# Kernel optimization log

Measured on AMD Instinct MI355X. Metric: run time of the kernel, lower is better.

The kernel has to match this reference:

```python
import jax, jax.numpy as jnp
import numpy as np

B, T, D, H, C = 32, 512, 768, 512, 7


def setup_inputs() -> dict:
    key = jax.random.key(0)
    ks = jax.random.split(key, 10)
    g = lambda k, shape: jax.random.normal(k, shape, jnp.float32) * 0.02
    return {
        "x": jax.random.normal(ks[0], (B, T, D), jnp.float32),
        # PyTorch LSTM params; b = b_ih + b_hh folded into one bias (same math)
        "Wf_ih": g(ks[1], (4 * H, 2 * D)),
        "Wf_hh": g(ks[2], (4 * H, H)),
        "bf": jnp.zeros((4 * H,), jnp.float32),
        "Wb_ih": g(ks[3], (4 * H, 2 * D)),
        "Wb_hh": g(ks[4], (4 * H, H)),
        "bb": jnp.zeros((4 * H,), jnp.float32),
        "W_enc": g(ks[5], (H, D)),
        "b_enc": jnp.zeros((H,), jnp.float32),
        "W_dec": g(ks[6], (H, H)),
        "b_dec": jnp.zeros((H,), jnp.float32),
        "v": jax.random.uniform(ks[7], (H,), jnpp := jnp.float32) if False else jax.random.uniform(ks[7], (H,), jnp.float32),
        "W_head": g(ks[8], (C, 2 * H)),
        "b_head": jnp.zeros((C,), jnp.float32),
    }


def reference(x, Wf_ih, Wf_hh, bf, Wb_ih, Wb_hh, bb, W_enc, b_enc, W_dec, b_dec, v, W_head, b_head):
    hid = W_dec.shape[0]
    # encoder projection is time-invariant -> hoist out of the loop (same math as original)
    enc_proj = jnp.einsum('btd,hd->bth', x, W_enc) + b_enc  # (B,T,H)

    def run_direction(x_seq, Wih, Whh, b):
        def step(carry, xt):
            h, c = carry                                    # (B,H) each
            dec = h @ W_dec.T + b_dec                       # (B,H)
            scores = jnp.tanh(enc_proj + dec[:, None, :]) @ v  # (B,T)
            w = jax.nn.softmax(scores, axis=1)
            ctx = jnp.einsum('bt,btd->bd', w, x)            # (B,D)
            inp = jnp.concatenate([ctx, xt], axis=1)        # (B,2D)
            gates = inp @ Wih.T + h @ Whh.T + b             # (B,4H), torch order i,f,g,o
            i_, f_, g_, o_ = jnp.split(gates, 4, axis=1)
            c = jax.nn.sigmoid(f_) * c + jax.nn.sigmoid(i_) * jnp.tanh(g_)
            h = jax.nn.sigmoid(o_) * jnp.tanh(c)
            return (h, c), h

        h0 = jnp.zeros((x.shape[0], hid), x.dtype)
        (_, _), hs = jax.lax.scan(step, (h0, h0), x_seq)
        return hs                                           # (T,B,H)

    x_seq = jnp.swapaxes(x, 0, 1)                           # (T,B,D)
    hs_f = run_direction(x_seq, Wf_ih, Wf_hh, bf)
    hs_b = run_direction(x_seq[::-1], Wb_ih, Wb_hh, bb)[::-1]
    comb = jnp.swapaxes(jnp.concatenate([hs_f, hs_b], axis=-1), 0, 1)  # (B,T,2H)
    return comb @ W_head.T + b_head                          # (B,T,C)
```

## Files before the change

### kernel.cpp

```cpp
#include <hip/hip_runtime.h>
#include <cstdint>
#include <cstddef>

#define L2E 1.4426950408889634f

typedef __attribute__((ext_vector_type(8))) short short8v;
typedef __attribute__((ext_vector_type(4))) float f32x4;
typedef unsigned long long ull;

__device__ __forceinline__ float fexp2(float x){ return __builtin_amdgcn_exp2f(x); }
__device__ __forceinline__ float frcp(float x){ return __builtin_amdgcn_rcpf(x); }
__device__ __forceinline__ float tanh_f(float x){
  return 1.f - 2.f*frcp(1.f + fexp2(2.f*L2E*x));
}
__device__ __forceinline__ float sigm_f(float x){
  return frcp(1.f + fexp2(-L2E*x));
}
__device__ __forceinline__ float bf2f(ushort u){ return __uint_as_float(((uint32_t)u)<<16); }
__device__ __forceinline__ ushort f2bf(float f){
  uint32_t x = __float_as_uint(f);
  uint32_t r = (x + 0x7FFFu + ((x>>16)&1u)) >> 16;
  return (ushort)r;
}

__device__ __forceinline__ float ld4f(const float* p){
  return __hip_atomic_load((float*)p, __ATOMIC_RELAXED, __HIP_MEMORY_SCOPE_AGENT);
}
__device__ __forceinline__ void st4f(float* p, float v){
  __hip_atomic_store(p, v, __ATOMIC_RELAXED, __HIP_MEMORY_SCOPE_AGENT);
}
__device__ __forceinline__ float2 ld8f(const float* p){
  union { ull u; float2 f; } c;
  c.u = __hip_atomic_load((ull*)p, __ATOMIC_RELAXED, __HIP_MEMORY_SCOPE_AGENT);
  return c.f;
}
__device__ __forceinline__ short8v ld16h(const ushort* p){
  union { ull u[2]; short8v s; } c;
  c.u[0] = __hip_atomic_load((ull*)p,     __ATOMIC_RELAXED, __HIP_MEMORY_SCOPE_AGENT);
  c.u[1] = __hip_atomic_load((ull*)(p+4), __ATOMIC_RELAXED, __HIP_MEMORY_SCOPE_AGENT);
  return c.s;
}
__device__ __forceinline__ void st8u(ushort* p, ull v){
  __hip_atomic_store((ull*)p, v, __ATOMIC_RELAXED, __HIP_MEMORY_SCOPE_AGENT);
}

namespace {
constexpr int NB = 32, TT = 512, DD = 768, HH = 512;
constexpr size_t EPB  = 0;
constexpr size_t XBB  = EPB  + (size_t)NB*HH*TT*2;
constexpr size_t HSB  = XBB  + (size_t)NB*TT*DD*2;
constexpr size_t WPKB = HSB  + (size_t)2*TT*NB*HH*2;
constexpr size_t WDPB = WPKB + (size_t)2*128*64*64*8*2;
constexpr size_t UCTXB= WDPB + (size_t)32*16*64*8*2;
constexpr size_t ZBB  = UCTXB+ (size_t)2*NB*DD*4;
constexpr size_t DECB = ZBB  + (size_t)2*NB*4;
constexpr size_t CSTB = DECB + (size_t)2*NB*HH*4;
constexpr size_t GSYB = CSTB + (size_t)2*NB*HH*4;
constexpr size_t WS_BYTES = GSYB + 32768;

constexpr int EPL  = 0;
constexpr int WPL  = 65536;
constexpr int REDL = 131072;
constexpr int DC2L = 147456;
constexpr int VSML = 151552;
constexpr int SCRL = 153600;
constexpr int EVSL = 157696;
constexpr int GFNL = 158208;
constexpr int LDS_BYTES = GFNL + 2176;
}

__device__ __forceinline__ void bar_arrive(uint* flags, uint token, int bid){
  __syncthreads();
  if (threadIdx.x == 0)
    __hip_atomic_store(&flags[bid*16], token, __ATOMIC_RELAXED, __HIP_MEMORY_SCOPE_AGENT);
}
__device__ __forceinline__ void bar_wait(uint* flags, uint token){
  if (threadIdx.x < 256) {
    while (__hip_atomic_load(&flags[threadIdx.x*16], __ATOMIC_RELAXED, __HIP_MEMORY_SCOPE_AGENT) < token)
      __builtin_amdgcn_s_sleep(1);
  }
  __syncthreads();
  asm volatile("" ::: "memory");
}

__global__ void k_xcast(const float* __restrict__ x, ushort* __restrict__ xb)
{
  size_t i = ((size_t)blockIdx.x*256 + threadIdx.x)*8;
  float4 v0 = *(const float4*)(x + i);
  float4 v1 = *(const float4*)(x + i + 4);
  short8v o;
  o[0]=(short)f2bf(v0.x); o[1]=(short)f2bf(v0.y); o[2]=(short)f2bf(v0.z); o[3]=(short)f2bf(v0.w);
  o[4]=(short)f2bf(v1.x); o[5]=(short)f2bf(v1.y); o[6]=(short)f2bf(v1.z); o[7]=(short)f2bf(v1.w);
  *(short8v*)(xb + i) = o;
}

__global__ void k_encproj(const float* __restrict__ x, const float* __restrict__ Wenc,
                          const float* __restrict__ benc, ushort* __restrict__ epT)
{
  int b = blockIdx.z, h0 = blockIdx.y*64, t0 = blockIdx.x*64;
  __shared__ float As[64][33];
  __shared__ float Bs[64][33];
  int tid = threadIdx.x;
  int n = tid & 63, mg = tid >> 6;
  float acc[16];
  #pragma unroll
  for (int j = 0; j < 16; j++) acc[j] = 0.f;
  int lr = tid >> 2, lk = (tid & 3) * 8;
  for (int k0 = 0; k0 < 768; k0 += 32) {
    const float* ap = Wenc + (size_t)(h0 + lr)*768 + k0 + lk;
    #pragma unroll
    for (int i = 0; i < 8; i++) As[lr][lk + i] = ap[i];
    const float* bp = x + ((size_t)b*512 + t0 + lr)*768 + k0 + lk;
    #pragma unroll
    for (int i = 0; i < 8; i++) Bs[lr][lk + i] = bp[i];
    __syncthreads();
    #pragma unroll
    for (int kk = 0; kk < 32; kk++) {
      float bv = Bs[n][kk];
      #pragma unroll
      for (int j = 0; j < 16; j++) acc[j] += As[mg*16 + j][kk] * bv;
    }
    __syncthreads();
  }
  #pragma unroll
  for (int j = 0; j < 16; j++) {
    int h = h0 + mg*16 + j;
    epT[((size_t)b*512 + h)*512 + t0 + n] = f2bf(acc[j] + benc[h]);
  }
}

__global__ void k_wpack(const float* __restrict__ Wfih, const float* __restrict__ Wfhh,
                        const float* __restrict__ Wbih, const float* __restrict__ Wbhh,
                        ushort* __restrict__ wpk)
{
  size_t f = (size_t)blockIdx.x*256 + threadIdx.x;
  int lane = (int)(f & 63), kstep = (int)((f>>6)&63), jblk = (int)((f>>12)&127), dir = (int)(f>>19);
  const float* Whh = dir ? Wbhh : Wfhh;
  const float* Wih = dir ? Wbih : Wfih;
  int c = lane & 15, gate = c >> 2, jj = c & 3;
  int row = gate*512 + jblk*4 + jj;
  int kbase = kstep*32 + (lane>>4)*8;
  short8v o;
  #pragma unroll
  for (int i = 0; i < 8; i++) {
    int k = kbase + i;
    float w = (k < 512) ? Whh[(size_t)row*512 + k] : Wih[(size_t)row*1536 + (k - 512)];
    o[i] = (short)f2bf(w);
  }
  *(short8v*)(wpk + f*8) = o;
}

__global__ void k_wdpack(const float* __restrict__ Wdec, ushort* __restrict__ wdp)
{
  int f = blockIdx.x*256 + threadIdx.x;
  int lane = f & 63, kstep = (f >> 6) & 15, nb = f >> 10;
  int n = nb*16 + (lane & 15);
  int kbase = kstep*32 + (lane >> 4)*8;
  short8v o;
  #pragma unroll
  for (int i = 0; i < 8; i++) o[i] = (short)f2bf(Wdec[(size_t)n*512 + kbase + i]);
  *(short8v*)(wdp + (size_t)f*8) = o;
}

__device__ __forceinline__ void gates_hx(int s, int wid, int lane, int l15, int lk8, int dirG,
    const ushort* __restrict__ hsb, const ushort* __restrict__ xb,
    const ushort* wpk_l, float* RED)
{
  if (wid >= 2 && wid <= 4) return;
  int b0 = l15, b1 = 16 + l15;
  f32x4 acc0 = {0,0,0,0}, acc1 = {0,0,0,0};
  if (wid < 2) {
    if (s > 0) {
      int t_prev = dirG ? (512 - s) : (s - 1);
      const ushort* h0 = hsb + (((size_t)dirG*512 + t_prev)*32 + b0)*512;
      const ushort* h1 = hsb + (((size_t)dirG*512 + t_prev)*32 + b1)*512;
      #pragma unroll
      for (int kk = 0; kk < 8; kk++) {
        int kstep = wid*8 + kk;
        int ko = kstep*32 + lk8;
        short8v a0v = ld16h(h0 + ko);
        short8v a1v = ld16h(h1 + ko);
        short8v bv  = *(const short8v*)(wpk_l + (size_t)kstep*512 + lane*8);
        acc0 = __builtin_amdgcn_mfma_f32_16x16x32_bf16(a0v, bv, acc0, 0, 0, 0);
        acc1 = __builtin_amdgcn_mfma_f32_16x16x32_bf16(a1v, bv, acc1, 0, 0, 0);
      }
    }
  } else {
    int t_in = dirG ? (511 - s) : s;
    const ushort* x0 = xb + ((size_t)b0*512 + t_in)*768;
    const ushort* x1 = xb + ((size_t)b1*512 + t_in)*768;
    #pragma unroll
    for (int kk = 0; kk < 8; kk++) {
      int kstep = wid*8 + kk;
      int ko = kstep*32 - 1280 + lk8;
      short8v a0v = __builtin_nontemporal_load((const short8v*)(x0 + ko));
      short8v a1v = __builtin_nontemporal_load((const short8v*)(x1 + ko));
      short8v bv  = *(const short8v*)(wpk_l + (size_t)kstep*512 + lane*8);
      acc0 = __builtin_amdgcn_mfma_f32_16x16x32_bf16(a0v, bv, acc0, 0, 0, 0);
      acc1 = __builtin_amdgcn_mfma_f32_16x16x32_bf16(a1v, bv, acc1, 0, 0, 0);
    }
  }
  int rr = (lane >> 4) * 4;
  #pragma unroll
  for (int r = 0; r < 4; r++) RED[((size_t)wid*32 + rr + r)*16 + l15] = acc0[r];
  #pragma unroll
  for (int r = 0; r < 4; r++) RED[((size_t)wid*32 + 16 + rr + r)*16 + l15] = acc1[r];
}

__global__ __launch_bounds__(512, 1) void k_loop(
    ushort* __restrict__ hsb, const ushort* __restrict__ xb, const ushort* __restrict__ ep,
    const ushort* __restrict__ wpk, const ushort* __restrict__ wdp,
    float* __restrict__ uctx, float* __restrict__ Zb, float* __restrict__ dec,
    float* __restrict__ cst, const float* __restrict__ bdec, const float* __restrict__ vg,
    const float* __restrict__ bfv, const float* __restrict__ bbv,
    uint* __restrict__ flags)
{
  extern __shared__ __align__(16) char dsm[];
  ushort* ep_l  = (ushort*)(dsm + EPL);
  ushort* wpk_l = (ushort*)(dsm + WPL);
  float*  RED   = (float*)(dsm + REDL);
  float*  DEC2  = (float*)(dsm + DC2L);
  float*  VSM   = (float*)(dsm + VSML);
  float*  SCRS  = (float*)(dsm + SCRL);
  float*  EVS   = (float*)(dsm + EVSL);
  float*  GFIN  = (float*)(dsm + GFNL);

  const int bid = blockIdx.x;
  const int tid = threadIdx.x;
  const int wid = tid >> 6, lane = tid & 63;
  const int l15 = lane & 15, lk8 = (lane >> 4) * 8;
  const int bS = bid >> 3, t0 = (bid & 7) * 64;
  const int dirG = bid >> 7, jblkG = bid & 127;
  uint bar_t = 0;

  {
    const ushort* esrc = ep + ((size_t)bS*512)*512 + t0;
    for (int i = tid; i < 4096; i += 512) {
      int h = i >> 3, c = i & 7;
      *(short8v*)(ep_l + h*64 + c*8) = *(const short8v*)(esrc + (size_t)h*512 + c*8);
    }
    const ushort* wsrc = wpk + (((size_t)dirG*128 + jblkG)*64)*512;
    for (int i = tid; i < 4096; i += 512)
      ((short8v*)wpk_l)[i] = ((const short8v*)wsrc)[i];
    VSM[tid] = vg[tid];
  }
  __syncthreads();

  for (int s = 0; s < TT; ++s) {
    if (bid < 32) {
      int nb = bid;
      if (s == 0) {
        for (int e = tid; e < 1024; e += 512) {
          int row = e >> 4, col = e & 15;
          st4f(dec + (size_t)row*512 + nb*16 + col, bdec[nb*16 + col]);
        }
      } else {
        f32x4 acc[4] = {{0,0,0,0},{0,0,0,0},{0,0,0,0},{0,0,0,0}};
        int tp0 = s - 1, tp1 = 512 - s;
        #pragma unroll
        for (int kk = 0; kk < 2; kk++) {
          int kstep = wid*2 + kk;
          int ko = kstep*32 + lk8;
          short8v bv = *(const short8v*)(wdp + (((size_t)nb*16 + kstep)*64 + lane)*8);
          #pragma unroll
          for (int m = 0; m < 4; m++) {
            int dir = m >> 1, brow = (m & 1)*16 + l15;
            int tp = dir ? tp1 : tp0;
            short8v av = ld16h(hsb + (((size_t)dir*512 + tp)*32 + brow)*512 + ko);
            acc[m] = __builtin_amdgcn_mfma_f32_16x16x32_bf16(av, bv, acc[m], 0, 0, 0);
          }
        }
        int rr = (lane >> 4) * 4;
        #pragma unroll
        for (int pass = 0; pass < 2; pass++) {
          #pragma unroll
          for (int mh = 0; mh < 2; mh++)
            #pragma unroll
            for (int r = 0; r < 4; r++)
              RED[((size_t)wid*32 + mh*16 + rr + r)*16 + l15] = acc[pass*2 + mh][r];
          __syncthreads();
          {
            int row = tid >> 4, col = tid & 15;
            float dv = 0.f;
            #pragma unroll
            for (int w = 0; w < 8; w++) dv += RED[((size_t)w*32 + row)*16 + col];
            st4f(dec + ((size_t)pass*32 + row)*512 + nb*16 + col, dv + bdec[nb*16 + col]);
          }
          __syncthreads();
        }
      }
    } else if (bid < 64) {
      int base = (bid - 32)*512 + tid;
      for (int i = base; i < 2*32*768; i += 16384) st4f(uctx + i, 0.f);
      if (base < 64) st4f(Zb + base, 0.f);
    }
    ++bar_t; bar_arrive(flags, bar_t, bid);
    gates_hx(s, wid, lane, l15, lk8, dirG, hsb, xb, wpk_l, RED);
    bar_wait(flags, bar_t);

    {
      DEC2[tid]       = ld4f(dec + (size_t)bS*512 + tid);
      DEC2[512 + tid] = ld4f(dec + ((size_t)32 + bS)*512 + tid);
      __syncthreads();
      int tl = tid & 63, hg = tid >> 6;
      float s0 = 0.f, s1 = 0.f;
      #pragma unroll 8
      for (int hh = 0; hh < 64; hh++) {
        int h = hg*64 + hh;
        float e = bf2f(ep_l[(size_t)h*64 + tl]);
        float vv = VSM[h];
        s0 += tanh_f(e + DEC2[h]) * vv;
        s1 += tanh_f(e + DEC2[512 + h]) * vv;
      }
      SCRS[((size_t)0*8 + hg)*64 + tl] = s0;
      SCRS[((size_t)1*8 + hg)*64 + tl] = s1;
      __syncthreads();
      if (tid < 128) {
        int dq = tid >> 6, tq = tid & 63;
        float sv = 0.f;
        #pragma unroll
        for (int g = 0; g < 8; g++) sv += SCRS[((size_t)dq*8 + g)*64 + tq];
        sv = fminf(sv, 100.f);
        float e = fexp2((sv - 32.f)*L2E);
        EVS[dq*64 + tq] = e;
        float z = e;
        #pragma unroll
        for (int off = 32; off; off >>= 1) z += __shfl_xor(z, off);
        if (tq == 0) unsafeAtomicAdd(Zb + dq*32 + bS, z);
      }
      __syncthreads();
      for (int dd = tid; dd < 768; dd += 512) {
        const ushort* xp = xb + ((size_t)bS*512 + t0)*768 + dd;
        float a0 = 0.f, a1 = 0.f;
        #pragma unroll 8
        for (int t = 0; t < 64; t++) {
          float xv = bf2f(xp[(size_t)t*768]);
          a0 += EVS[t]*xv;
          a1 += EVS[64 + t]*xv;
        }
        unsafeAtomicAdd(uctx + (size_t)bS*768 + dd, a0);
        unsafeAtomicAdd(uctx + ((size_t)32 + bS)*768 + dd, a1);
      }
    }
    ++bar_t; bar_arrive(flags, bar_t, bid);
    bar_wait(flags, bar_t);

    {
      if (wid >= 2 && wid <= 4) {
        int b0 = l15, b1 = 16 + l15;
        f32x4 acc0 = {0,0,0,0}, acc1 = {0,0,0,0};
        float zi0 = 1.0f / ld4f(Zb + dirG*32 + b0);
        float zi1 = 1.0f / ld4f(Zb + dirG*32 + b1);
        const float* u0 = uctx + ((size_t)dirG*32 + b0)*768;
        const float* u1 = uctx + ((size_t)dirG*32 + b1)*768;
        #pragma unroll
        for (int kk = 0; kk < 8; kk++) {
          int kstep = wid*8 + kk;
          int ko = kstep*32 - 512 + lk8;
          float2 xa = ld8f(u0 + ko),     xc = ld8f(u0 + ko + 2);
          float2 xe = ld8f(u0 + ko + 4), xg = ld8f(u0 + ko + 6);
          float2 ya = ld8f(u1 + ko),     yc = ld8f(u1 + ko + 2);
          float2 ye = ld8f(u1 + ko + 4), yg = ld8f(u1 + ko + 6);
          short8v a0v, a1v;
          a0v[0]=(short)f2bf(xa.x*zi0); a0v[1]=(short)f2bf(xa.y*zi0);
          a0v[2]=(short)f2bf(xc.x*zi0); a0v[3]=(short)f2bf(xc.y*zi0);
          a0v[4]=(short)f2bf(xe.x*zi0); a0v[5]=(short)f2bf(xe.y*zi0);
          a0v[6]=(short)f2bf(xg.x*zi0); a0v[7]=(short)f2bf(xg.y*zi0);
          a1v[0]=(short)f2bf(ya.x*zi1); a1v[1]=(short)f2bf(ya.y*zi1);
          a1v[2]=(short)f2bf(yc.x*zi1); a1v[3]=(short)f2bf(yc.y*zi1);
          a1v[4]=(short)f2bf(ye.x*zi1); a1v[5]=(short)f2bf(ye.y*zi1);
          a1v[6]=(short)f2bf(yg.x*zi1); a1v[7]=(short)f2bf(yg.y*zi1);
          short8v bv = *(const short8v*)(wpk_l + (size_t)kstep*512 + lane*8);
          acc0 = __builtin_amdgcn_mfma_f32_16x16x32_bf16(a0v, bv, acc0, 0, 0, 0);
          acc1 = __builtin_amdgcn_mfma_f32_16x16x32_bf16(a1v, bv, acc1, 0, 0, 0);
        }
        int rr = (lane >> 4) * 4;
        #pragma unroll
        for (int r = 0; r < 4; r++) RED[((size_t)wid*32 + rr + r)*16 + l15] = acc0[r];
        #pragma unroll
        for (int r = 0; r < 4; r++) RED[((size_t)wid*32 + 16 + rr + r)*16 + l15] = acc1[r];
      }
      __syncthreads();
      {
        int bb = tid >> 4, c = tid & 15;
        float g = 0.f;
        #pragma unroll
        for (int w = 0; w < 8; w++) g += RED[((size_t)w*32 + bb)*16 + c];
        GFIN[bb*17 + c] = g;
      }
      __syncthreads();
      if (tid < 32) {
        int b = tid;
        int j0 = jblkG*4;
        const float* bias = dirG ? bbv : bfv;
        size_t ci0 = ((size_t)dirG*32 + b)*512 + j0;
        float4 co = *(const float4*)&cst[ci0];
        float cold[4] = {co.x, co.y, co.z, co.w};
        float4 cn4;
        ull hp = 0;
        #pragma unroll
        for (int jj = 0; jj < 4; jj++) {
          int j = j0 + jj;
          float gi  = GFIN[b*17 + jj]       + bias[j];
          float gf  = GFIN[b*17 + 4 + jj]   + bias[512 + j];
          float gg  = GFIN[b*17 + 8 + jj]   + bias[1024 + j];
          float go_ = GFIN[b*17 + 12 + jj]  + bias[1536 + j];
          float cn = sigm_f(gf)*cold[jj] + sigm_f(gi)*tanh_f(gg);
          float h  = sigm_f(go_)*tanh_f(cn);
          ((float*)&cn4)[jj] = cn;
          hp |= ((ull)f2bf(h)) << (16*jj);
        }
        *(float4*)&cst[ci0] = cn4;
        int tw = dirG ? (511 - s) : s;
        st8u(hsb + (((size_t)dirG*512 + tw)*32 + b)*512 + j0, hp);
      }
    }
    ++bar_t; bar_arrive(flags, bar_t, bid);
    bar_wait(flags, bar_t);
  }
}

__global__ void k_head(const ushort* __restrict__ hsb, const float* __restrict__ Wh,
                       const float* __restrict__ bh, float* __restrict__ out)
{
  int wid = threadIdx.x >> 6, lane = threadIdx.x & 63;
  int r = blockIdx.x*4 + wid;
  int b = r >> 9, t = r & 511;
  float acc[7];
  #pragma unroll
  for (int c = 0; c < 7; c++) acc[c] = 0.f;
  const ushort* hf = hsb + (((size_t)t)*32 + b)*512;
  const ushort* hb = hsb + (((size_t)512 + t)*32 + b)*512;
  for (int k0 = 0; k0 < 512; k0 += 64) {
    int k = k0 + lane;
    float a = bf2f(hf[k]), bvv = bf2f(hb[k]);
    #pragma unroll
    for (int c = 0; c < 7; c++)
      acc[c] += a*Wh[c*1024 + k] + bvv*Wh[c*1024 + 512 + k];
  }
  #pragma unroll
  for (int c = 0; c < 7; c++) {
    float sres = acc[c];
    #pragma unroll
    for (int off = 32; off; off >>= 1) sres += __shfl_xor(sres, off);
    if (lane == c) out[((size_t)b*512 + t)*7 + c] = sres + bh[c];
  }
}

extern "C" void kernel_launch(void* const* d_in, const int* in_sizes, int n_in,
                              void* d_out, int out_size, void* d_ws, size_t ws_size,
                              hipStream_t stream) {
  (void)in_sizes; (void)n_in; (void)out_size;
  const float* x    = (const float*)d_in[0];
  const float* Wfih = (const float*)d_in[1];
  const float* Wfhh = (const float*)d_in[2];
  const float* bfv  = (const float*)d_in[3];
  const float* Wbih = (const float*)d_in[4];
  const float* Wbhh = (const float*)d_in[5];
  const float* bbv  = (const float*)d_in[6];
  const float* Wenc = (const float*)d_in[7];
  const float* benc = (const float*)d_in[8];
  const float* Wdec = (const float*)d_in[9];
  const float* bdec = (const float*)d_in[10];
  const float* v    = (const float*)d_in[11];
  const float* Whead= (const float*)d_in[12];
  const float* bhead= (const float*)d_in[13];
  float* out = (float*)d_out;
  char* ws = (char*)d_ws;

  if (ws_size < WS_BYTES) return;

  ushort* ep   = (ushort*)(ws + EPB);
  ushort* xb   = (ushort*)(ws + XBB);
  ushort* hsb  = (ushort*)(ws + HSB);
  ushort* wpk  = (ushort*)(ws + WPKB);
  ushort* wdp  = (ushort*)(ws + WDPB);
  float*  uctx = (float*)(ws + UCTXB);
  float*  Zb   = (float*)(ws + ZBB);
  float*  dec  = (float*)(ws + DECB);
  float*  cst  = (float*)(ws + CSTB);
  uint*   flags= (uint*)(ws + GSYB);

  hipFuncSetAttribute(reinterpret_cast<const void*>(k_loop),
                      hipFuncAttributeMaxDynamicSharedMemorySize, LDS_BYTES);

  hipMemsetAsync(ws + CSTB, 0, (size_t)2*NB*HH*4, stream);
  hipMemsetAsync(ws + GSYB, 0, 32768, stream);

  hipLaunchKernelGGL(k_xcast, dim3(6144), dim3(256), 0, stream, x, xb);
  hipLaunchKernelGGL(k_encproj, dim3(8,8,32), dim3(256), 0, stream, x, Wenc, benc, ep);
  hipLaunchKernelGGL(k_wpack, dim3(4096), dim3(256), 0, stream, Wfih, Wfhh, Wbih, Wbhh, wpk);
  hipLaunchKernelGGL(k_wdpack, dim3(128), dim3(256), 0, stream, Wdec, wdp);

  void* args[] = {
    (void*)&hsb, (void*)&xb, (void*)&ep, (void*)&wpk, (void*)&wdp,
    (void*)&uctx, (void*)&Zb, (void*)&dec, (void*)&cst,
    (void*)&bdec, (void*)&v, (void*)&bfv, (void*)&bbv, (void*)&flags
  };
  hipLaunchCooperativeKernel(reinterpret_cast<void*>(k_loop), dim3(256), dim3(512),
                             args, LDS_BYTES, stream);

  hipLaunchKernelGGL(k_head, dim3(4096), dim3(256), 0, stream, hsb, Whead, bhead, out);
}
```

Before: 15.48 ms.

## Repartition attention by hidden chunks with group-local sync, drop a grid barrier

Each block now owns a 64-wide hidden chunk for one batch row instead of a 64-step time slice. It computes its slice of the decoder projection redundantly, writes partial attention scores, and syncs only with the 8 blocks of its batch through new group flags. Those blocks then do the softmax and context reduction locally and write a normalized bf16 context, which removes one grid-wide barrier per step along with the global atomics on uctx and Zb. The cost is redundant decoder-projection work done with scalar FMAs instead of MFMA, and a global scratch buffer that aliases the encoder-projection region after it has been copied into LDS.

Result: slower. 16.11 ms (+4.0%).

```diff
diff --git a/kernel.cpp b/kernel.cpp
--- a/kernel.cpp
+++ b/kernel.cpp
@@ -29,10 +29,8 @@
 __device__ __forceinline__ void st4f(float* p, float v){
   __hip_atomic_store(p, v, __ATOMIC_RELAXED, __HIP_MEMORY_SCOPE_AGENT);
 }
-__device__ __forceinline__ float2 ld8f(const float* p){
-  union { ull u; float2 f; } c;
-  c.u = __hip_atomic_load((ull*)p, __ATOMIC_RELAXED, __HIP_MEMORY_SCOPE_AGENT);
-  return c.f;
+__device__ __forceinline__ void st2h(ushort* p, ushort v){
+  __hip_atomic_store(p, v, __ATOMIC_RELAXED, __HIP_MEMORY_SCOPE_AGENT);
 }
 __device__ __forceinline__ short8v ld16h(const ushort* p){
   union { ull u[2]; short8v s; } c;
@@ -61,11 +59,12 @@
 constexpr int EPL  = 0;
 constexpr int WPL  = 65536;
 constexpr int REDL = 131072;
-constexpr int DC2L = 147456;
-constexpr int VSML = 151552;
-constexpr int SCRL = 153600;
-constexpr int EVSL = 157696;
-constexpr int GFNL = 158208;
+constexpr int HEVL = 147456;
+constexpr int DPL  = 151552;
+constexpr int DECL = 153600;
+constexpr int VVL  = 154112;
+constexpr int CSCL = 154368;
+constexpr int GFNL = 157440;
 constexpr int LDS_BYTES = GFNL + 2176;
 }
 
@@ -75,9 +74,12 @@
     __hip_atomic_store(&flags[bid*16], token, __ATOMIC_RELAXED, __HIP_MEMORY_SCOPE_AGENT);
 }
 __device__ __forceinline__ void bar_wait(uint* flags, uint token){
-  if (threadIdx.x < 256) {
-    while (__hip_atomic_load(&flags[threadIdx.x*16], __ATOMIC_RELAXED, __HIP_MEMORY_SCOPE_AGENT) < token)
-      __builtin_amdgcn_s_sleep(1);
+  if (threadIdx.x < 64) {
+    #pragma unroll
+    for (int j = 0; j < 4; j++) {
+      while (__hip_atomic_load(&flags[(threadIdx.x*4 + j)*16], __ATOMIC_RELAXED, __HIP_MEMORY_SCOPE_AGENT) < token)
+        __builtin_amdgcn_s_sleep(1);
+    }
   }
   __syncthreads();
   asm volatile("" ::: "memory");
@@ -210,167 +212,167 @@
 __global__ __launch_bounds__(512, 1) void k_loop(
     ushort* __restrict__ hsb, const ushort* __restrict__ xb, const ushort* __restrict__ ep,
     const ushort* __restrict__ wpk, const ushort* __restrict__ wdp,
-    float* __restrict__ uctx, float* __restrict__ Zb, float* __restrict__ dec,
+    float* __restrict__ spart, ushort* __restrict__ ctxf,
     float* __restrict__ cst, const float* __restrict__ bdec, const float* __restrict__ vg,
     const float* __restrict__ bfv, const float* __restrict__ bbv,
-    uint* __restrict__ flags)
+    uint* __restrict__ flags, uint* __restrict__ gfl)
 {
   extern __shared__ __align__(16) char dsm[];
   ushort* ep_l  = (ushort*)(dsm + EPL);
   ushort* wpk_l = (ushort*)(dsm + WPL);
   float*  RED   = (float*)(dsm + REDL);
-  float*  DEC2  = (float*)(dsm + DC2L);
-  float*  VSM   = (float*)(dsm + VSML);
-  float*  SCRS  = (float*)(dsm + SCRL);
-  float*  EVS   = (float*)(dsm + EVSL);
+  float*  HEV   = (float*)(dsm + HEVL);
+  float*  DP    = (float*)(dsm + DPL);
+  float*  DEC   = (float*)(dsm + DECL);
+  float*  VV    = (float*)(dsm + VVL);
+  float*  CSC   = (float*)(dsm + CSCL);
   float*  GFIN  = (float*)(dsm + GFNL);
 
   const int bid = blockIdx.x;
   const int tid = threadIdx.x;
   const int wid = tid >> 6, lane = tid & 63;
   const int l15 = lane & 15, lk8 = (lane >> 4) * 8;
-  const int bS = bid >> 3, t0 = (bid & 7) * 64;
+  const int bS = bid >> 3, hc = bid & 7;
   const int dirG = bid >> 7, jblkG = bid & 127;
   uint bar_t = 0;
 
   {
-    const ushort* esrc = ep + ((size_t)bS*512)*512 + t0;
-    for (int i = tid; i < 4096; i += 512) {
-      int h = i >> 3, c = i & 7;
-      *(short8v*)(ep_l + h*64 + c*8) = *(const short8v*)(esrc + (size_t)h*512 + c*8);
-    }
-    const ushort* wsrc = wpk + (((size_t)dirG*128 + jblkG)*64)*512;
-    for (int i = tid; i < 4096; i += 512)
-      ((short8v*)wpk_l)[i] = ((const short8v*)wsrc)[i];
-    VSM[tid] = vg[tid];
-  }
-  __syncthreads();
+    const short8v* esrc = (const short8v*)(ep + ((size_t)bS*512 + hc*64)*512);
+    short8v* edst = (short8v*)ep_l;
+    for (int i = tid; i < 4096; i += 512) edst[i] = esrc[i];
+    const short8v* wsrc = (const short8v*)(wpk + (((size_t)dirG*128 + jblkG)*64)*512);
+    short8v* wdst = (short8v*)wpk_l;
+    for (int i = tid; i < 4096; i += 512) wdst[i] = wsrc[i];
+    if (tid < 64) VV[tid] = vg[hc*64 + tid];
+  }
+  ++bar_t; bar_arrive(flags, bar_t, bid); bar_wait(flags, bar_t);
 
   for (int s = 0; s < TT; ++s) {
-    if (bid < 32) {
-      int nb = bid;
-      if (s == 0) {
-        for (int e = tid; e < 1024; e += 512) {
-          int row = e >> 4, col = e & 15;
-          st4f(dec + (size_t)row*512 + nb*16 + col, bdec[nb*16 + col]);
+    if (s == 0) {
+      if (tid < 128) { int dir = tid >> 6, n = tid & 63; DEC[dir*64 + n] = bdec[hc*64 + n]; }
+    } else {
+      if (tid < 128) {
+        int dir = tid >> 6, q = tid & 63;
+        int tp = dir ? (512 - s) : (s - 1);
+        short8v hv = ld16h(hsb + (((size_t)dir*512 + tp)*32 + bS)*512 + q*8);
+        #pragma unroll
+        for (int j = 0; j < 8; j++) HEV[dir*512 + q*8 + j] = bf2f((ushort)hv[j]);
+      }
+      __syncthreads();
+      {
+        int dir = tid >> 8, n = (tid >> 2) & 63, kq = tid & 3;
+        int ng = hc*64 + n;
+        int nb = ng >> 4, c = ng & 15;
+        const float* hrow = HEV + dir*512 + kq*128;
+        float a = 0.f;
+        #pragma unroll
+        for (int ch = 0; ch < 16; ch++) {
+          int kstep = kq*4 + (ch >> 2);
+          int lhi = ch & 3;
+          short8v w8 = *(const short8v*)(wdp + (((size_t)nb*16 + kstep)*64 + lhi*16 + c)*8);
+          #pragma unroll
+          for (int j = 0; j < 8; j++) a += bf2f((ushort)w8[j]) * hrow[ch*8 + j];
         }
-      } else {
-        f32x4 acc[4] = {{0,0,0,0},{0,0,0,0},{0,0,0,0},{0,0,0,0}};
-        int tp0 = s - 1, tp1 = 512 - s;
-        #pragma unroll
-        for (int kk = 0; kk < 2; kk++) {
-          int kstep = wid*2 + kk;
-          int ko = kstep*32 + lk8;
-          short8v bv = *(const short8v*)(wdp + (((size_t)nb*16 + kstep)*64 + lane)*8);
-          #pragma unroll
-          for (int m = 0; m < 4; m++) {
-            int dir = m >> 1, brow = (m & 1)*16 + l15;
-            int tp = dir ? tp1 : tp0;
-            short8v av = ld16h(hsb + (((size_t)dir*512 + tp)*32 + brow)*512 + ko);
-            acc[m] = __builtin_amdgcn_mfma_f32_16x16x32_bf16(av, bv, acc[m], 0, 0, 0);
-          }
-        }
-        int rr = (lane >> 4) * 4;
-        #pragma unroll
-        for (int pass = 0; pass < 2; pass++) {
-          #pragma unroll
-          for (int mh = 0; mh < 2; mh++)
-            #pragma unroll
-            for (int r = 0; r < 4; r++)
-              RED[((size_t)wid*32 + mh*16 + rr + r)*16 + l15] = acc[pass*2 + mh][r];
-          __syncthreads();
-          {
-            int row = tid >> 4, col = tid & 15;
-            float dv = 0.f;
-            #pragma unroll
-            for (int w = 0; w < 8; w++) dv += RED[((size_t)w*32 + row)*16 + col];
-            st4f(dec + ((size_t)pass*32 + row)*512 + nb*16 + col, dv + bdec[nb*16 + col]);
-          }
-          __syncthreads();
-        }
-      }
-    } else if (bid < 64) {
-      int base = (bid - 32)*512 + tid;
-      for (int i = base; i < 2*32*768; i += 16384) st4f(uctx + i, 0.f);
-      if (base < 64) st4f(Zb + base, 0.f);
-    }
+        DP[tid] = a;
+      }
+      __syncthreads();
+      if (tid < 128) {
+        int dir = tid >> 6, n = tid & 63;
+        const float* dp = DP + dir*256 + n*4;
+        DEC[dir*64 + n] = dp[0] + dp[1] + dp[2] + dp[3] + bdec[hc*64 + n];
+      }
+    }
+    __syncthreads();
+
+    {
+      int t = tid;
+      float s0 = 0.f, s1 = 0.f;
+      #pragma unroll 8
+      for (int h = 0; h < 64; h++) {
+        float e = bf2f(ep_l[h*512 + t]);
+        float vv = VV[h];
+        s0 += tanh_f(e + DEC[h]) * vv;
+        s1 += tanh_f(e + DEC[64 + h]) * vv;
+      }
+      float* sp = spart + (((size_t)(bS*8 + hc))*2)*512;
+      st4f(sp + t, s0);
+      st4f(sp + 512 + t, s1);
+    }
+    __syncthreads();
+    if (tid == 0)
+      __hip_atomic_store(&gfl[bid*16], (uint)(s + 1), __ATOMIC_RELAXED, __HIP_MEMORY_SCOPE_AGENT);
+    if (tid < 8) {
+      while (__hip_atomic_load(&gfl[(bS*8 + tid)*16], __ATOMIC_RELAXED, __HIP_MEMORY_SCOPE_AGENT) < (uint)(s + 1))
+        __builtin_amdgcn_s_sleep(1);
+    }
+    __syncthreads();
+
+    {
+      int t = tid;
+      float s0 = 0.f, s1 = 0.f;
+      #pragma unroll
+      for (int j = 0; j < 8; j++) {
+        const float* sp = spart + (((size_t)(bS*8 + j))*2)*512;
+        s0 += ld4f(sp + t);
+        s1 += ld4f(sp + 512 + t);
+      }
+      s0 = fminf(s0, 100.f); s1 = fminf(s1, 100.f);
+      float e0 = fexp2((s0 - 32.f)*L2E);
+      float e1 = fexp2((s1 - 32.f)*L2E);
+      HEV[t] = e0; HEV[512 + t] = e1;
+      float z0 = e0, z1 = e1;
+      #pragma unroll
+      for (int off = 32; off; off >>= 1) { z0 += __shfl_xor(z0, off); z1 += __shfl_xor(z1, off); }
+      if (lane == 0) { DP[wid] = z0; DP[8 + wid] = z1; }
+    }
+    __syncthreads();
+    if (tid < 2) {
+      float z = 0.f;
+      const float* zp = DP + tid*8;
+      #pragma unroll
+      for (int w = 0; w < 8; w++) z += zp[w];
+      DP[128 + tid] = frcp(z);
+    }
+    __syncthreads();
+
+    if (tid < 384) {
+      int dl = tid % 96, tq = tid / 96;
+      const ushort* xp = xb + (((size_t)bS*512 + tq*128)*768) + hc*96 + dl;
+      float a0 = 0.f, a1 = 0.f;
+      #pragma unroll 8
+      for (int t2 = 0; t2 < 128; t2++) {
+        float xv = bf2f(xp[(size_t)t2*768]);
+        a0 += HEV[tq*128 + t2]*xv;
+        a1 += HEV[512 + tq*128 + t2]*xv;
+      }
+      CSC[(dl*2 + 0)*4 + tq] = a0;
+      CSC[(dl*2 + 1)*4 + tq] = a1;
+    }
+    __syncthreads();
+    if (tid < 192) {
+      int dl = tid % 96, dir = tid / 96;
+      const float* cp = CSC + (dl*2 + dir)*4;
+      float cv = (cp[0] + cp[1] + cp[2] + cp[3]) * DP[128 + dir];
+      st2h(ctxf + ((size_t)dir*32 + bS)*768 + hc*96 + dl, f2bf(cv));
+    }
+
     ++bar_t; bar_arrive(flags, bar_t, bid);
     gates_hx(s, wid, lane, l15, lk8, dirG, hsb, xb, wpk_l, RED);
-    bar_wait(flags, bar_t);
-
-    {
-      DEC2[tid]       = ld4f(dec + (size_t)bS*512 + tid);
-      DEC2[512 + tid] = ld4f(dec + ((size_t)32 + bS)*512 + tid);
-      __syncthreads();
-      int tl = tid & 63, hg = tid >> 6;
-      float s0 = 0.f, s1 = 0.f;
-      #pragma unroll 8
-      for (int hh = 0; hh < 64; hh++) {
-        int h = hg*64 + hh;
-        float e = bf2f(ep_l[(size_t)h*64 + tl]);
-        float vv = VSM[h];
-        s0 += tanh_f(e + DEC2[h]) * vv;
-        s1 += tanh_f(e + DEC2[512 + h]) * vv;
-      }
-      SCRS[((size_t)0*8 + hg)*64 + tl] = s0;
-      SCRS[((size_t)1*8 + hg)*64 + tl] = s1;
-      __syncthreads();
-      if (tid < 128) {
-        int dq = tid >> 6, tq = tid & 63;
-        float sv = 0.f;
-        #pragma unroll
-        for (int g = 0; g < 8; g++) sv += SCRS[((size_t)dq*8 + g)*64 + tq];
-        sv = fminf(sv, 100.f);
-        float e = fexp2((sv - 32.f)*L2E);
-        EVS[dq*64 + tq] = e;
-        float z = e;
-        #pragma unroll
-        for (int off = 32; off; off >>= 1) z += __shfl_xor(z, off);
-        if (tq == 0) unsafeAtomicAdd(Zb + dq*32 + bS, z);
-      }
-      __syncthreads();
-      for (int dd = tid; dd < 768; dd += 512) {
-        const ushort* xp = xb + ((size_t)bS*512 + t0)*768 + dd;
-        float a0 = 0.f, a1 = 0.f;
-        #pragma unroll 8
-        for (int t = 0; t < 64; t++) {
-          float xv = bf2f(xp[(size_t)t*768]);
-          a0 += EVS[t]*xv;
-          a1 += EVS[64 + t]*xv;
-        }
-        unsafeAtomicAdd(uctx + (size_t)bS*768 + dd, a0);
-        unsafeAtomicAdd(uctx + ((size_t)32 + bS)*768 + dd, a1);
-      }
-    }
-    ++bar_t; bar_arrive(flags, bar_t, bid);
     bar_wait(flags, bar_t);
 
     {
       if (wid >= 2 && wid <= 4) {
         int b0 = l15, b1 = 16 + l15;
         f32x4 acc0 = {0,0,0,0}, acc1 = {0,0,0,0};
-        float zi0 = 1.0f / ld4f(Zb + dirG*32 + b0);
-        float zi1 = 1.0f / ld4f(Zb + dirG*32 + b1);
-        const float* u0 = uctx + ((size_t)dirG*32 + b0)*768;
-        const float* u1 = uctx + ((size_t)dirG*32 + b1)*768;
+        const ushort* c0 = ctxf + ((size_t)dirG*32 + b0)*768;
+        const ushort* c1 = ctxf + ((size_t)dirG*32 + b1)*768;
         #pragma unroll
         for (int kk = 0; kk < 8; kk++) {
           int kstep = wid*8 + kk;
           int ko = kstep*32 - 512 + lk8;
-          float2 xa = ld8f(u0 + ko),     xc = ld8f(u0 + ko + 2);
-          float2 xe = ld8f(u0 + ko + 4), xg = ld8f(u0 + ko + 6);
-          float2 ya = ld8f(u1 + ko),     yc = ld8f(u1 + ko + 2);
-          float2 ye = ld8f(u1 + ko + 4), yg = ld8f(u1 + ko + 6);
-          short8v a0v, a1v;
-          a0v[0]=(short)f2bf(xa.x*zi0); a0v[1]=(short)f2bf(xa.y*zi0);
-          a0v[2]=(short)f2bf(xc.x*zi0); a0v[3]=(short)f2bf(xc.y*zi0);
-          a0v[4]=(short)f2bf(xe.x*zi0); a0v[5]=(short)f2bf(xe.y*zi0);
-          a0v[6]=(short)f2bf(xg.x*zi0); a0v[7]=(short)f2bf(xg.y*zi0);
-          a1v[0]=(short)f2bf(ya.x*zi1); a1v[1]=(short)f2bf(ya.y*zi1);
-          a1v[2]=(short)f2bf(yc.x*zi1); a1v[3]=(short)f2bf(yc.y*zi1);
-          a1v[4]=(short)f2bf(ye.x*zi1); a1v[5]=(short)f2bf(ye.y*zi1);
-          a1v[6]=(short)f2bf(yg.x*zi1); a1v[7]=(short)f2bf(yg.y*zi1);
-          short8v bv = *(const short8v*)(wpk_l + (size_t)kstep*512 + lane*8);
+          short8v a0v = ld16h(c0 + ko);
+          short8v a1v = ld16h(c1 + ko);
+          short8v bv  = *(const short8v*)(wpk_l + (size_t)kstep*512 + lane*8);
           acc0 = __builtin_amdgcn_mfma_f32_16x16x32_bf16(a0v, bv, acc0, 0, 0, 0);
           acc1 = __builtin_amdgcn_mfma_f32_16x16x32_bf16(a1v, bv, acc1, 0, 0, 0);
         }
@@ -471,15 +473,15 @@
   if (ws_size < WS_BYTES) return;
 
   ushort* ep   = (ushort*)(ws + EPB);
+  float*  spart= (float*)(ws + EPB);
   ushort* xb   = (ushort*)(ws + XBB);
   ushort* hsb  = (ushort*)(ws + HSB);
   ushort* wpk  = (ushort*)(ws + WPKB);
   ushort* wdp  = (ushort*)(ws + WDPB);
-  float*  uctx = (float*)(ws + UCTXB);
-  float*  Zb   = (float*)(ws + ZBB);
-  float*  dec  = (float*)(ws + DECB);
+  ushort* ctxf = (ushort*)(ws + UCTXB);
   float*  cst  = (float*)(ws + CSTB);
   uint*   flags= (uint*)(ws + GSYB);
+  uint*   gfl  = (uint*)(ws + GSYB + 16384);
 
   hipFuncSetAttribute(reinterpret_cast<const void*>(k_loop),
                       hipFuncAttributeMaxDynamicSharedMemorySize, LDS_BYTES);
@@ -494,8 +496,8 @@
 
   void* args[] = {
     (void*)&hsb, (void*)&xb, (void*)&ep, (void*)&wpk, (void*)&wdp,
-    (void*)&uctx, (void*)&Zb, (void*)&dec, (void*)&cst,
-    (void*)&bdec, (void*)&v, (void*)&bfv, (void*)&bbv, (void*)&flags
+    (void*)&spart, (void*)&ctxf, (void*)&cst,
+    (void*)&bdec, (void*)&v, (void*)&bfv, (void*)&bbv, (void*)&flags, (void*)&gfl
   };
   hipLaunchCooperativeKernel(reinterpret_cast<void*>(k_loop), dim3(256), dim3(512),
                              args, LDS_BYTES, stream);
```
